# Kernel tuning notes

Measured on AMD Instinct MI355X. Metric: run time of the kernel, lower is better.

Reference implementation:

```python
import jax, jax.numpy as jnp
import numpy as np

N_NODES = 50000
N_EDGES = 800000
DIM = 64
N_LAYERS = 5


def setup_inputs() -> dict:
    key = jax.random.key(0)
    k1, k2, k3, k4, k5 = jax.random.split(key, 5)
    x = jax.random.normal(k1, (N_NODES, DIM), dtype=jnp.float32)
    # 3 weight matrices per GIN layer (2 hidden + 1 output Dense, all [dim,dim], relu, no bias)
    W = jax.random.normal(k2, (N_LAYERS, 3, DIM, DIM), dtype=jnp.float32) * (1.0 / np.sqrt(DIM))
    # per-layer read-out Dense(1, use_bias=False)
    Wl = jax.random.normal(k3, (N_LAYERS, DIM), dtype=jnp.float32) * (1.0 / np.sqrt(DIM))
    src = jax.random.randint(k4, (N_EDGES,), 0, N_NODES, dtype=jnp.int32)
    dst = jax.random.randint(k5, (N_EDGES,), 0, N_NODES, dtype=jnp.int32)
    return {"x": x, "W": W, "Wl": Wl, "src": src, "dst": dst}


def reference(x, W, Wl, src, dst):
    n = x.shape[0]
    h = x
    pooled = []  # per-layer global mean pool  [dim]
    for i in range(N_LAYERS):
        agg = h + jax.ops.segment_sum(h[src], dst, num_segments=n)  # (1+eps)*h + sum_neighbors
        h = jax.nn.relu(agg @ W[i, 0])
        h = jax.nn.relu(h @ W[i, 1])
        h = jax.nn.relu(h @ W[i, 2])
        pooled.append(jnp.mean(h, axis=0))
    # stack per-layer Dense(1) read-outs, sum over layers, sigmoid -> shape [1]
    logits = jnp.einsum("ld,ld->l", jnp.stack(pooled), Wl)  # [5]
    return jax.nn.sigmoid(jnp.sum(logits)[None])
```

## Files before the change

kernel.cpp:

```cpp
#include <hip/hip_runtime.h>
#include <hip/hip_fp16.h>
#include <math.h>

#define N_NODES 50000
#define N_EDGES 800000
#define DIM 64
#define N_LAYERS 5

#define BLK 256
#define ROWS 32
#define HSTRIDE 68
#define POOL_REP 16

#define CAP 64
#define NB 196
#define NROW_PAD (NB * 256)
#define CAPB 5632
#define BF_BLOCKS 512
#define EPB2 ((N_EDGES + BF_BLOCKS - 1) / BF_BLOCKS)

#define WFRAG_PER_LAYER (3 * 2 * 4 * 64 * 8)
#define XP (N_NODES * DIM / 4)
#define WP (N_LAYERS * WFRAG_PER_LAYER)
#define PREP_BLOCKS ((XP + WP) / 256)

typedef __attribute__((ext_vector_type(8))) short short8;
typedef __attribute__((ext_vector_type(8))) unsigned short ushort8_t;
typedef __attribute__((ext_vector_type(4))) float floatx4;

__device__ inline unsigned short bf16_rne(float f) {
    unsigned int u = __float_as_uint(f);
    return (unsigned short)((u + 0x7FFFu + ((u >> 16) & 1u)) >> 16);
}
__device__ inline float e5m2_f32(unsigned char b) {
    return __half2float(__ushort_as_half((unsigned short)((unsigned short)b << 8)));
}
__device__ inline unsigned char f32_e5m2(float f) {
    unsigned short us = __half_as_ushort(__float2half(f));
    us = (unsigned short)(us + 0x7F + ((us >> 8) & 1));
    return (unsigned char)(us >> 8);
}
__device__ inline __half2 e5m2x2_lo(unsigned d) {
    unsigned h = __builtin_amdgcn_perm(0u, d, 0x01050004u);
    return __builtin_bit_cast(__half2, h);
}
__device__ inline __half2 e5m2x2_hi(unsigned d) {
    unsigned h = __builtin_amdgcn_perm(0u, d, 0x03070206u);
    return __builtin_bit_cast(__half2, h);
}

__global__ __launch_bounds__(256) void setup_kernel(const float* __restrict__ x,
                                                    const float* __restrict__ W,
                                                    const int* __restrict__ src,
                                                    const int* __restrict__ dst,
                                                    unsigned char* __restrict__ x8,
                                                    unsigned short* __restrict__ wfrag,
                                                    int* __restrict__ bucketCnt,
                                                    int* __restrict__ ebuf) {
    __shared__ int cnt[NB];
    __shared__ int basev[NB];
    int b = blockIdx.x;
    const int t = threadIdx.x;
    if (b < PREP_BLOCKS) {
        int i = b * 256 + t;
        if (i < XP) {
            float4 v = ((const float4*)x)[i];
            uchar4 u;
            u.x = f32_e5m2(v.x); u.y = f32_e5m2(v.y);
            u.z = f32_e5m2(v.z); u.w = f32_e5m2(v.w);
            ((uchar4*)x8)[i] = u;
        } else {
            int tt = i - XP;
            int j    = tt & 7;
            int lane = (tt >> 3) & 63;
            int nt   = (tt >> 9) & 3;
            int kt   = (tt >> 11) & 1;
            int rest = tt >> 12;
            int p    = rest % 3;
            int layer= rest / 3;
            int k = kt * 32 + (lane >> 4) * 8 + j;
            int n = nt * 16 + (lane & 15);
            float v = W[(((size_t)layer * 3 + p) * 64 + k) * 64 + n];
            wfrag[tt] = bf16_rne(v);
        }
        return;
    }
    b -= PREP_BLOCKS;
    const int e0 = b * EPB2;
    for (int j = t; j < NB; j += 256) cnt[j] = 0;
    __syncthreads();
    for (int i = t; i < EPB2; i += 256) {
        int e = e0 + i;
        if (e < N_EDGES) atomicAdd(&cnt[dst[e] >> 8], 1);
    }
    __syncthreads();
    for (int j = t; j < NB; j += 256) {
        int c = cnt[j];
        basev[j] = c ? atomicAdd(&bucketCnt[j], c) : 0;
        cnt[j] = 0;
    }
    __syncthreads();
    for (int i = t; i < EPB2; i += 256) {
        int e = e0 + i;
        if (e < N_EDGES) {
            int d = dst[e];
            int bb = d >> 8;
            int pos = atomicAdd(&cnt[bb], 1);
            ebuf[(size_t)bb * CAPB + basev[bb] + pos] = ((d & 255) << 16) | src[e];
        }
    }
}

__global__ __launch_bounds__(512) void bell_kernel(const int* __restrict__ ebuf,
                                                   const int* __restrict__ bucketCnt,
                                                   int* __restrict__ rowCnt,
                                                   unsigned short* __restrict__ ell) {
    __shared__ int cur[256];
    __shared__ unsigned short tile[256 * CAP];
    const int t = threadIdx.x;
    const int b = blockIdx.x;
    const int cnt_b = min(bucketCnt[b], CAPB);
    const int* __restrict__ ereg = ebuf + (size_t)b * CAPB;

    if (t < 256) cur[t] = 0;
    __syncthreads();
    for (int i = t; i < cnt_b; i += 512) {
        int e = ereg[i];
        int r = (e >> 16) & 255;
        int pos = atomicAdd(&cur[r], 1);
        if (pos < CAP)
            tile[r * CAP + pos] = (unsigned short)(e & 0xFFFF);
    }
    __syncthreads();
    if (t < 256) rowCnt[b * 256 + t] = min(cur[t], CAP);
    uint4* eo = (uint4*)(ell + (size_t)b * 256 * CAP);
    const uint4* ti = (const uint4*)tile;
    #pragma unroll
    for (int j = 0; j < 4; ++j)
        eo[t + j * 512] = ti[t + j * 512];
}

__global__ __launch_bounds__(BLK) void layer_kernel(const unsigned char* __restrict__ h8,
                                                    const int* __restrict__ rowCnt,
                                                    const unsigned short* __restrict__ ell,
                                                    const unsigned short* __restrict__ wf,
                                                    unsigned char* __restrict__ h_out,
                                                    float* __restrict__ pooled) {
    __shared__ float H[ROWS * HSTRIDE];
    const int tid  = threadIdx.x;
    const int lane = tid & 63;
    const int w    = __builtin_amdgcn_readfirstlane(tid >> 6);
    const int n0   = blockIdx.x * ROWS;
    const int nw8  = n0 + w * 8;
    const int o8   = (lane & 7) << 3;
    const int rg   = lane >> 3;

    {
        const int cv = rowCnt[nw8 + (lane & 7)];
        const int deg = min(__shfl(cv, rg, 64), CAP);
        int Rm = deg;
        Rm = max(Rm, __shfl_xor(Rm, 8, 64));
        Rm = max(Rm, __shfl_xor(Rm, 16, 64));
        Rm = max(Rm, __shfl_xor(Rm, 32, 64));
        const int Rpad = (Rm + 7) & ~7;
        const int rowq = nw8 + rg;
        const int rq6  = rowq << 6;
        const unsigned short* ep = ell + ((size_t)rowq << 6);

        __half2 a01 = __float2half2_rn(0.f);
        __half2 a23 = a01, a45 = a01, a67 = a01;

        for (int i = 0; i < Rpad; i += 8) {
            ushort8_t ev = *(const ushort8_t*)(ep + i);
            uint2 dv[8];
            #pragma unroll
            for (int k = 0; k < 8; ++k) {
                int s6 = ((int)ev[k]) << 6;
                s6 = (i + k < deg) ? s6 : rq6;
                dv[k] = *(const uint2*)(h8 + (unsigned)(s6 | o8));
            }
            #pragma unroll
            for (int k = 0; k < 8; ++k) {
                a01 = __hadd2(a01, e5m2x2_lo(dv[k].x));
                a23 = __hadd2(a23, e5m2x2_hi(dv[k].x));
                a45 = __hadd2(a45, e5m2x2_lo(dv[k].y));
                a67 = __hadd2(a67, e5m2x2_hi(dv[k].y));
            }
        }

        uint2 sd = *(const uint2*)(h8 + (unsigned)(rq6 | o8));
        float scale = (float)(1 - (Rpad - deg));
        float2 f01 = __half22float2(a01), f23 = __half22float2(a23);
        float2 f45 = __half22float2(a45), f67 = __half22float2(a67);
        float4 r0, r1;
        r0.x = f01.x + e5m2_f32((unsigned char)(sd.x      )) * scale;
        r0.y = f01.y + e5m2_f32((unsigned char)(sd.x >>  8)) * scale;
        r0.z = f23.x + e5m2_f32((unsigned char)(sd.x >> 16)) * scale;
        r0.w = f23.y + e5m2_f32((unsigned char)(sd.x >> 24)) * scale;
        r1.x = f45.x + e5m2_f32((unsigned char)(sd.y      )) * scale;
        r1.y = f45.y + e5m2_f32((unsigned char)(sd.y >>  8)) * scale;
        r1.z = f67.x + e5m2_f32((unsigned char)(sd.y >> 16)) * scale;
        r1.w = f67.y + e5m2_f32((unsigned char)(sd.y >> 24)) * scale;
        if (rowq >= N_NODES) {
            r0.x = 0.f; r0.y = 0.f; r0.z = 0.f; r0.w = 0.f;
            r1.x = 0.f; r1.y = 0.f; r1.z = 0.f; r1.w = 0.f;
        }
        float* hp = &H[(w * 8 + rg) * HSTRIDE + o8];
        *(float4*)hp = r0;
        *(float4*)(hp + 4) = r1;
    }
    __syncthreads();

    if (w < 2) {
        const int mrow = lane & 15;
        const int quad = lane >> 4;
        const short8* Bf = (const short8*)wf;

        for (int p = 0; p < 3; ++p) {
            short8 Ahi[2];
            #pragma unroll
            for (int kt = 0; kt < 2; ++kt) {
                const float* ap = &H[(w * 16 + mrow) * HSTRIDE + kt * 32 + quad * 8];
                float4 f0 = *(const float4*)ap;
                float4 f1 = *(const float4*)(ap + 4);
                float fv[8] = {f0.x, f0.y, f0.z, f0.w, f1.x, f1.y, f1.z, f1.w};
                short8 hi;
                #pragma unroll
                for (int jj = 0; jj < 8; ++jj)
                    hi[jj] = (short)bf16_rne(fv[jj]);
                Ahi[kt] = hi;
            }

            floatx4 acc[4];
            #pragma unroll
            for (int nt = 0; nt < 4; ++nt) { acc[nt][0]=0.f; acc[nt][1]=0.f; acc[nt][2]=0.f; acc[nt][3]=0.f; }

            #pragma unroll
            for (int nt = 0; nt < 4; ++nt) {
                #pragma unroll
                for (int kt = 0; kt < 2; ++kt) {
                    int fbase = ((p * 2 + kt) * 4 + nt) * 64 + lane;
                    short8 bhi = Bf[fbase];
                    acc[nt] = __builtin_amdgcn_mfma_f32_16x16x32_bf16(Ahi[kt], bhi, acc[nt], 0, 0, 0);
                }
            }
            #pragma unroll
            for (int nt = 0; nt < 4; ++nt) {
                #pragma unroll
                for (int reg = 0; reg < 4; ++reg) {
                    int row = w * 16 + quad * 4 + reg;
                    H[row * HSTRIDE + nt * 16 + mrow] = fmaxf(acc[nt][reg], 0.f);
                }
            }
        }
    }
    __syncthreads();

    #pragma unroll
    for (int i = 0; i < 2; ++i) {
        int t4 = tid + i * BLK;
        int r  = t4 >> 4;
        int c  = (t4 & 15) << 2;
        int grow = n0 + r;
        if (grow < N_NODES) {
            float4 v = *(const float4*)&H[r * HSTRIDE + c];
            uchar4 u;
            u.x = f32_e5m2(v.x); u.y = f32_e5m2(v.y);
            u.z = f32_e5m2(v.z); u.w = f32_e5m2(v.w);
            *(uchar4*)(h_out + (size_t)grow * DIM + c) = u;
        }
    }

    if (tid < 64) {
        float s = 0.f;
        #pragma unroll
        for (int r = 0; r < ROWS; ++r)
            s += H[r * HSTRIDE + tid];
        atomicAdd(&pooled[(blockIdx.x & (POOL_REP - 1)) * DIM + tid], s);
    }
}

__global__ void finalize_kernel(const float* __restrict__ pooled,
                                const float* __restrict__ Wl,
                                float* __restrict__ out) {
    int c = threadIdx.x;
    float s = 0.f;
    #pragma unroll
    for (int l = 0; l < N_LAYERS; ++l) {
        float col = 0.f;
        #pragma unroll
        for (int r = 0; r < POOL_REP; ++r)
            col += pooled[(l * POOL_REP + r) * DIM + c];
        s += col * Wl[l * DIM + c];
    }
    #pragma unroll
    for (int off = 32; off > 0; off >>= 1)
        s += __shfl_down(s, off, 64);
    if (c == 0) {
        float logit = s / (float)N_NODES;
        out[0] = 1.f / (1.f + expf(-logit));
    }
}

extern "C" void kernel_launch(void* const* d_in, const int* in_sizes, int n_in,
                              void* d_out, int out_size, void* d_ws, size_t ws_size,
                              hipStream_t stream) {
    const float* x   = (const float*)d_in[0];
    const float* W   = (const float*)d_in[1];
    const float* Wl  = (const float*)d_in[2];
    const int*   src = (const int*)d_in[3];
    const int*   dst = (const int*)d_in[4];
    float* out = (float*)d_out;

    char* ws = (char*)d_ws;
    const size_t h8Bytes = (size_t)N_NODES * DIM;
    unsigned char* hX = (unsigned char*)(ws);
    unsigned char* hA = (unsigned char*)(ws + h8Bytes);
    unsigned char* hB = (unsigned char*)(ws + 2 * h8Bytes);
    unsigned short* ell = (unsigned short*)(ws + 3 * h8Bytes);
    int*   ebuf     = (int*)(ell + (size_t)NROW_PAD * CAP);
    int*   rowCnt   = ebuf + (size_t)NB * CAPB;
    int*   bucketCnt= rowCnt + NROW_PAD;
    float* pooled   = (float*)(bucketCnt + 256);
    unsigned short* wfrag = (unsigned short*)(pooled + N_LAYERS * POOL_REP * DIM);

    hipMemsetAsync(bucketCnt, 0, (256 + N_LAYERS * POOL_REP * DIM) * sizeof(int), stream);

    setup_kernel<<<PREP_BLOCKS + BF_BLOCKS, 256, 0, stream>>>(x, W, src, dst, hX, wfrag, bucketCnt, ebuf);
    bell_kernel<<<NB, 512, 0, stream>>>(ebuf, bucketCnt, rowCnt, ell);

    const unsigned char* hcur = hX;
    unsigned char* hnext = hA;
    const int grid = (N_NODES + ROWS - 1) / ROWS;
    for (int l = 0; l < N_LAYERS; ++l) {
        layer_kernel<<<grid, BLK, 0, stream>>>(
            hcur, rowCnt, ell, wfrag + (size_t)l * WFRAG_PER_LAYER, hnext,
            pooled + (size_t)l * POOL_REP * DIM);
        hcur = hnext;
        hnext = (hnext == hA) ? hB : hA;
    }
    finalize_kernel<<<1, 64, 0, stream>>>(pooled, Wl, out);
}
```

Before: 181.9 us.

## Fuse five GIN layers and finalize into one persistent kernel with grid barrier

Replaces the five per-layer launches and the finalize launch with a single persistent kernel of 784 blocks. Each block processes up to two 32-row chunks per layer, and layers are separated by a hierarchical atomic grid barrier. The goal is to remove launch gaps and tail effects between layers. The barrier relies on all 784 blocks being co-resident (launch_bounds 4 per CU) and adds spin-wait cost and a risk of deadlock. Pool replication is raised to reduce atomic contention.

```diff
diff --git a/kernel.cpp b/kernel.cpp
--- a/kernel.cpp
+++ b/kernel.cpp
@@ -10,7 +10,7 @@
 #define BLK 256
 #define ROWS 32
 #define HSTRIDE 68
-#define POOL_REP 16
+#define POOL_REP 64
 
 #define CAP 64
 #define NB 196
@@ -18,6 +18,9 @@
 #define CAPB 5632
 #define BF_BLOCKS 512
 #define EPB2 ((N_EDGES + BF_BLOCKS - 1) / BF_BLOCKS)
+
+#define GRID_C 784
+#define NCHUNK 1563
 
 #define WFRAG_PER_LAYER (3 * 2 * 4 * 64 * 8)
 #define XP (N_NODES * DIM / 4)
@@ -140,17 +143,18 @@
         eo[t + j * 512] = ti[t + j * 512];
 }
 
-__global__ __launch_bounds__(BLK) void layer_kernel(const unsigned char* __restrict__ h8,
-                                                    const int* __restrict__ rowCnt,
-                                                    const unsigned short* __restrict__ ell,
-                                                    const unsigned short* __restrict__ wf,
-                                                    unsigned char* __restrict__ h_out,
-                                                    float* __restrict__ pooled) {
-    __shared__ float H[ROWS * HSTRIDE];
+__device__ __forceinline__ void layer_chunk(const int v,
+                                            const unsigned char* __restrict__ h8,
+                                            const int* __restrict__ rowCnt,
+                                            const unsigned short* __restrict__ ell,
+                                            const unsigned short* __restrict__ wf,
+                                            unsigned char* __restrict__ h_out,
+                                            float* __restrict__ pooled,
+                                            float* H) {
     const int tid  = threadIdx.x;
     const int lane = tid & 63;
     const int w    = __builtin_amdgcn_readfirstlane(tid >> 6);
-    const int n0   = blockIdx.x * ROWS;
+    const int n0   = v * ROWS;
     const int nw8  = n0 + w * 8;
     const int o8   = (lane & 7) << 3;
     const int rg   = lane >> 3;
@@ -230,11 +234,9 @@
                     hi[jj] = (short)bf16_rne(fv[jj]);
                 Ahi[kt] = hi;
             }
-
             floatx4 acc[4];
             #pragma unroll
             for (int nt = 0; nt < 4; ++nt) { acc[nt][0]=0.f; acc[nt][1]=0.f; acc[nt][2]=0.f; acc[nt][3]=0.f; }
-
             #pragma unroll
             for (int nt = 0; nt < 4; ++nt) {
                 #pragma unroll
@@ -263,42 +265,82 @@
         int c  = (t4 & 15) << 2;
         int grow = n0 + r;
         if (grow < N_NODES) {
-            float4 v = *(const float4*)&H[r * HSTRIDE + c];
+            float4 vv = *(const float4*)&H[r * HSTRIDE + c];
             uchar4 u;
-            u.x = f32_e5m2(v.x); u.y = f32_e5m2(v.y);
-            u.z = f32_e5m2(v.z); u.w = f32_e5m2(v.w);
+            u.x = f32_e5m2(vv.x); u.y = f32_e5m2(vv.y);
+            u.z = f32_e5m2(vv.z); u.w = f32_e5m2(vv.w);
             *(uchar4*)(h_out + (size_t)grow * DIM + c) = u;
         }
     }
-
     if (tid < 64) {
         float s = 0.f;
         #pragma unroll
         for (int r = 0; r < ROWS; ++r)
             s += H[r * HSTRIDE + tid];
-        atomicAdd(&pooled[(blockIdx.x & (POOL_REP - 1)) * DIM + tid], s);
-    }
-}
-
-__global__ void finalize_kernel(const float* __restrict__ pooled,
-                                const float* __restrict__ Wl,
-                                float* __restrict__ out) {
-    int c = threadIdx.x;
-    float s = 0.f;
-    #pragma unroll
+        atomicAdd(&pooled[(v & (POOL_REP - 1)) * DIM + tid], s);
+    }
+}
+
+__device__ __forceinline__ void gbar2(int* bar, int gen) {
+    __syncthreads();
+    if (threadIdx.x == 0) {
+        const int grp = blockIdx.x & 3;
+        int c = __hip_atomic_fetch_add(&bar[grp * 32], 1, __ATOMIC_RELEASE, __HIP_MEMORY_SCOPE_AGENT);
+        if (c == 196 * (gen + 1) - 1) {
+            int r = __hip_atomic_fetch_add(&bar[128], 1, __ATOMIC_ACQ_REL, __HIP_MEMORY_SCOPE_AGENT);
+            if (r == 4 * (gen + 1) - 1)
+                __hip_atomic_store(&bar[160], gen + 1, __ATOMIC_RELEASE, __HIP_MEMORY_SCOPE_AGENT);
+        }
+        while (__hip_atomic_load(&bar[160], __ATOMIC_RELAXED, __HIP_MEMORY_SCOPE_AGENT) < gen + 1)
+            __builtin_amdgcn_s_sleep(64);
+    }
+    __syncthreads();
+    __threadfence();
+}
+
+__global__ __launch_bounds__(BLK, 4) void gin5_kernel(const unsigned char* __restrict__ hX,
+                                                      unsigned char* __restrict__ hA,
+                                                      unsigned char* __restrict__ hB,
+                                                      const int* __restrict__ rowCnt,
+                                                      const unsigned short* __restrict__ ell,
+                                                      const unsigned short* __restrict__ wfrag,
+                                                      float* __restrict__ pooled,
+                                                      int* __restrict__ bar,
+                                                      const float* __restrict__ Wl,
+                                                      float* __restrict__ out) {
+    __shared__ float H[ROWS * HSTRIDE];
+    const int b = blockIdx.x;
+
     for (int l = 0; l < N_LAYERS; ++l) {
-        float col = 0.f;
+        const unsigned char* hc = (l == 0) ? hX : ((l & 1) ? hA : hB);
+        unsigned char* hn = (l & 1) ? hB : hA;
+        const unsigned short* wf = wfrag + (size_t)l * WFRAG_PER_LAYER;
+        float* pl = pooled + (size_t)l * POOL_REP * DIM;
+
+        layer_chunk(b, hc, rowCnt, ell, wf, hn, pl, H);
+        __syncthreads();
+        if (b + GRID_C < NCHUNK)
+            layer_chunk(b + GRID_C, hc, rowCnt, ell, wf, hn, pl, H);
+
+        gbar2(bar, l);
+    }
+
+    if (b == 0 && threadIdx.x < 64) {
+        int c = threadIdx.x;
+        float s = 0.f;
+        for (int l = 0; l < N_LAYERS; ++l) {
+            float col = 0.f;
+            for (int r = 0; r < POOL_REP; ++r)
+                col += pooled[(l * POOL_REP + r) * DIM + c];
+            s += col * Wl[l * DIM + c];
+        }
         #pragma unroll
-        for (int r = 0; r < POOL_REP; ++r)
-            col += pooled[(l * POOL_REP + r) * DIM + c];
-        s += col * Wl[l * DIM + c];
-    }
-    #pragma unroll
-    for (int off = 32; off > 0; off >>= 1)
-        s += __shfl_down(s, off, 64);
-    if (c == 0) {
-        float logit = s / (float)N_NODES;
-        out[0] = 1.f / (1.f + expf(-logit));
+        for (int off = 32; off > 0; off >>= 1)
+            s += __shfl_down(s, off, 64);
+        if (c == 0) {
+            float logit = s / (float)N_NODES;
+            out[0] = 1.f / (1.f + expf(-logit));
+        }
     }
 }
 
@@ -321,23 +363,13 @@
     int*   ebuf     = (int*)(ell + (size_t)NROW_PAD * CAP);
     int*   rowCnt   = ebuf + (size_t)NB * CAPB;
     int*   bucketCnt= rowCnt + NROW_PAD;
-    float* pooled   = (float*)(bucketCnt + 256);
+    int*   bar      = bucketCnt + 256;
+    float* pooled   = (float*)(bar + 256);
     unsigned short* wfrag = (unsigned short*)(pooled + N_LAYERS * POOL_REP * DIM);
 
-    hipMemsetAsync(bucketCnt, 0, (256 + N_LAYERS * POOL_REP * DIM) * sizeof(int), stream);
+    hipMemsetAsync(bucketCnt, 0, (256 + 256 + N_LAYERS * POOL_REP * DIM) * sizeof(int), stream);
 
     setup_kernel<<<PREP_BLOCKS + BF_BLOCKS, 256, 0, stream>>>(x, W, src, dst, hX, wfrag, bucketCnt, ebuf);
     bell_kernel<<<NB, 512, 0, stream>>>(ebuf, bucketCnt, rowCnt, ell);
-
-    const unsigned char* hcur = hX;
-    unsigned char* hnext = hA;
-    const int grid = (N_NODES + ROWS - 1) / ROWS;
-    for (int l = 0; l < N_LAYERS; ++l) {
-        layer_kernel<<<grid, BLK, 0, stream>>>(
-            hcur, rowCnt, ell, wfrag + (size_t)l * WFRAG_PER_LAYER, hnext,
-            pooled + (size_t)l * POOL_REP * DIM);
-        hcur = hnext;
-        hnext = (hnext == hA) ? hB : hA;
-    }
-    finalize_kernel<<<1, 64, 0, stream>>>(pooled, Wl, out);
-}
+    gin5_kernel<<<GRID_C, BLK, 0, stream>>>(hX, hA, hB, rowCnt, ell, wfrag, pooled, bar, Wl, out);
+}
```

New measurement: 483.8 us. 2.66x slower.
